# Kernel tuning notes

Hardware: AMD Instinct MI355X
Metric: run time of the kernel (lower is better)

Reference implementation:

```python
import jax, jax.numpy as jnp
import numpy as np

NUM_EMBEDDINGS = 1024
EMBEDDING_DIM = 128
COMMITMENT_COST = 0.25


def setup_inputs() -> dict:
    key = jax.random.key(0)
    k1, k2 = jax.random.split(key)
    z = jax.random.normal(k1, (16, EMBEDDING_DIM, 64, 64), dtype=jnp.float32)
    # torch init: uniform(-1/num_embeddings, 1/num_embeddings)
    lim = 1.0 / NUM_EMBEDDINGS
    embedding = jax.random.uniform(
        k2, (NUM_EMBEDDINGS, EMBEDDING_DIM), dtype=jnp.float32,
        minval=-lim, maxval=lim)
    return {"z": z, "embedding": embedding}


def reference(z, embedding):
    b, c, h, w = z.shape  # c == EMBEDDING_DIM
    # (b, h, w, c) -> (b*h*w, c)
    z_flat = jnp.transpose(z, (0, 2, 3, 1)).reshape(-1, c)
    # squared euclidean distances: ||z||^2 + ||e||^2 - 2 z e^T  -> (N, K)
    distances = (jnp.sum(z_flat ** 2, axis=-1, keepdims=True)
                 + jnp.sum(embedding ** 2, axis=-1)[None, :]
                 - 2.0 * jnp.matmul(z_flat, embedding.T))
    encoding_indices = jnp.argmin(distances, axis=-1)  # (N,) int
    z_q = embedding[encoding_indices].reshape(b, h, w, c)
    z_q = jnp.transpose(z_q, (0, 3, 1, 2))  # (b, c, h, w)
    commitment_loss = COMMITMENT_COST * jnp.sum(
        (jax.lax.stop_gradient(z_q) - z) ** 2)
    codebook_loss = jnp.sum((z_q - jax.lax.stop_gradient(z)) ** 2)
    loss = codebook_loss + commitment_loss
    # straight-through estimator
    z_q_st = z + jax.lax.stop_gradient(z_q - z)
    return (z_q_st, loss, encoding_indices, commitment_loss, codebook_loss)
```

## Files before the change

kernel.cpp:

```cpp
#include <hip/hip_runtime.h>
#include <hip/hip_bf16.h>

#define C 128
#define HW 4096
#define NPOS 65536
#define K 1024
#define MB 128
#define NBLK (NPOS/MB)
#define RS 136
#define RSB 272
#define CHK 64
#define NCH (K/CHK)
#define CHB (CHK*RSB)

#define ZQ_OFF 0
#define LOSS_OFF 8388608
#define IDX_OFF 8388609
#define COMMIT_OFF 8454145
#define CODE_OFF 8454146

#define WS_IMG_OFF 8192

typedef __bf16 bf16x8 __attribute__((ext_vector_type(8)));
typedef float f32x4 __attribute__((ext_vector_type(4)));

__global__ void vq_prep(const float* __restrict__ emb, unsigned char* __restrict__ img) {
    int k = blockIdx.x;
    int l = threadIdx.x;
    float v0 = emb[k * C + l];
    float v1 = emb[k * C + 64 + l];
    __hip_bfloat16 h0 = __float2bfloat16(v0);
    __hip_bfloat16 h1 = __float2bfloat16(v1);
    unsigned short* row = (unsigned short*)(img + (size_t)k * RSB);
    row[l] = *(unsigned short*)&h0;
    row[64 + l] = *(unsigned short*)&h1;
    float s = v0 * v0 + v1 * v1;
    #pragma unroll
    for (int off = 32; off; off >>= 1) s += __shfl_down(s, off);
    if (l == 0) *(float*)(img + (size_t)k * RSB + 256) = s + 1.0f;
}

__global__ __launch_bounds__(256, 2)
void vq_main(const float* __restrict__ z, const float* __restrict__ emb,
             const unsigned char* __restrict__ img,
             float* __restrict__ out, float* __restrict__ S) {
    __shared__ unsigned short zt[MB * RS];
    __shared__ unsigned short bbuf[2][CHK * RS];
    __shared__ unsigned int wbest[4][MB];
    __shared__ unsigned short idxs[MB];
    __shared__ float lred[4];

    const int t = threadIdx.x;
    const int w = t >> 6;
    const int lane = t & 63;
    const int nn = lane & 15;
    const int q = lane >> 4;

    const int blk = blockIdx.x;
    const int n0g = blk * MB;
    const int b = n0g >> 12;
    const int hw0 = n0g & (HW - 1);
    const float* zg = z + (size_t)b * C * HW + hw0;

    for (int j = w; j < 17; j += 4) {
        __builtin_amdgcn_global_load_lds(
            (const __attribute__((address_space(1))) unsigned int*)(img + j * 1024 + lane * 16),
            (__attribute__((address_space(3))) unsigned int*)((unsigned char*)bbuf[0] + j * 1024),
            16, 0, 0);
    }

    {
        int pos = t & (MB - 1);
        int c0b = (t >> 7) * 64;
        #pragma unroll
        for (int i = 0; i < 16; ++i) {
            int c0 = c0b + i * 4;
            float f0 = zg[(size_t)(c0 + 0) * HW + pos];
            float f1 = zg[(size_t)(c0 + 1) * HW + pos];
            float f2 = zg[(size_t)(c0 + 2) * HW + pos];
            float f3 = zg[(size_t)(c0 + 3) * HW + pos];
            __hip_bfloat16 h0 = __float2bfloat16(f0), h1 = __float2bfloat16(f1),
                           h2 = __float2bfloat16(f2), h3 = __float2bfloat16(f3);
            ushort4 pk;
            pk.x = *(unsigned short*)&h0; pk.y = *(unsigned short*)&h1;
            pk.z = *(unsigned short*)&h2; pk.w = *(unsigned short*)&h3;
            *(ushort4*)&zt[pos * RS + c0] = pk;
        }
    }
    __syncthreads();

    bf16x8 a[8][4];
    #pragma unroll
    for (int mt = 0; mt < 8; ++mt)
        #pragma unroll
        for (int ks = 0; ks < 4; ++ks)
            a[mt][ks] = *(bf16x8*)&zt[(mt * 16 + nn) * RS + ks * 32 + q * 8];

    unsigned int best[8][4];
    #pragma unroll
    for (int mt = 0; mt < 8; ++mt)
        #pragma unroll
        for (int r = 0; r < 4; ++r) best[mt][r] = 0xFFFFFFFFu;

    for (int ch = 0; ch < NCH; ++ch) {
        const int p = ch & 1;
        if (ch + 1 < NCH) {
            const unsigned char* src = img + (size_t)(ch + 1) * CHB;
            for (int j = w; j < 17; j += 4) {
                __builtin_amdgcn_global_load_lds(
                    (const __attribute__((address_space(1))) unsigned int*)(src + j * 1024 + lane * 16),
                    (__attribute__((address_space(3))) unsigned int*)((unsigned char*)bbuf[p ^ 1] + j * 1024),
                    16, 0, 0);
            }
        }
        const unsigned short* bb = bbuf[p];
        const int row = w * 16 + nn;
        bf16x8 bf[4];
        #pragma unroll
        for (int ks = 0; ks < 4; ++ks)
            bf[ks] = *(bf16x8*)&bb[row * RS + ks * 32 + q * 8];
        const float en1 = *(const float*)&bb[row * RS + 128];
        const unsigned int code = (unsigned int)(ch * CHK + row);

        f32x4 acc[8];
        #pragma unroll
        for (int mt = 0; mt < 8; ++mt) acc[mt] = (f32x4){0.f, 0.f, 0.f, 0.f};
        #pragma unroll
        for (int ks = 0; ks < 4; ++ks)
            #pragma unroll
            for (int mt = 0; mt < 8; ++mt)
                acc[mt] = __builtin_amdgcn_mfma_f32_16x16x32_bf16(a[mt][ks], bf[ks], acc[mt], 0, 0, 0);

        #pragma unroll
        for (int mt = 0; mt < 8; ++mt)
            #pragma unroll
            for (int r = 0; r < 4; ++r) {
                float s = fmaf(acc[mt][r], -2.0f, en1);
                unsigned int u = (__float_as_uint(s) & ~1023u) | code;
                best[mt][r] = min(best[mt][r], u);
            }
        __syncthreads();
    }

    #pragma unroll
    for (int mt = 0; mt < 8; ++mt)
        #pragma unroll
        for (int r = 0; r < 4; ++r) {
            unsigned int v = best[mt][r];
            v = min(v, (unsigned int)__shfl_xor((int)v, 1));
            v = min(v, (unsigned int)__shfl_xor((int)v, 2));
            v = min(v, (unsigned int)__shfl_xor((int)v, 4));
            v = min(v, (unsigned int)__shfl_xor((int)v, 8));
            if (nn == 0) wbest[w][mt * 16 + q * 4 + r] = v;
        }
    __syncthreads();

    if (t < MB) {
        unsigned int v = min(min(wbest[0][t], wbest[1][t]), min(wbest[2][t], wbest[3][t]));
        unsigned int code = v & 1023u;
        idxs[t] = (unsigned short)code;
        out[IDX_OFF + n0g + t] = (float)code;
    }
    __syncthreads();

    {
        int pos = t & (MB - 1);
        int c0b = (t >> 7) * 64;
        int myidx = idxs[pos];
        const float* erow = emb + (size_t)myidx * C;
        float* og = out + ZQ_OFF + (size_t)b * C * HW + hw0;
        float ls = 0.f;
        #pragma unroll
        for (int i = 0; i < 16; ++i) {
            int c0 = c0b + i * 4;
            float4 ev = *(const float4*)&erow[c0];
            ushort4 zz = *(ushort4*)&zt[pos * RS + c0];
            float z0 = __uint_as_float((unsigned int)zz.x << 16);
            float z1 = __uint_as_float((unsigned int)zz.y << 16);
            float z2 = __uint_as_float((unsigned int)zz.z << 16);
            float z3 = __uint_as_float((unsigned int)zz.w << 16);
            float d0 = z0 - ev.x, d1 = z1 - ev.y, d2 = z2 - ev.z, d3 = z3 - ev.w;
            ls += d0 * d0 + d1 * d1 + d2 * d2 + d3 * d3;
            og[(size_t)(c0 + 0) * HW + pos] = ev.x;
            og[(size_t)(c0 + 1) * HW + pos] = ev.y;
            og[(size_t)(c0 + 2) * HW + pos] = ev.z;
            og[(size_t)(c0 + 3) * HW + pos] = ev.w;
        }
        #pragma unroll
        for (int off = 32; off; off >>= 1) ls += __shfl_down(ls, off);
        if (lane == 0) lred[w] = ls;
    }
    __syncthreads();
    if (t == 0) atomicAdd(S, lred[0] + lred[1] + lred[2] + lred[3]);
}

__global__ void vq_final(const float* __restrict__ S, float* __restrict__ out) {
    float s = *S;
    out[LOSS_OFF] = 1.25f * s;
    out[COMMIT_OFF] = 0.25f * s;
    out[CODE_OFF] = s;
}

extern "C" void kernel_launch(void* const* d_in, const int* in_sizes, int n_in,
                              void* d_out, int out_size, void* d_ws, size_t ws_size,
                              hipStream_t stream) {
    const float* z = (const float*)d_in[0];
    const float* emb = (const float*)d_in[1];
    float* out = (float*)d_out;
    float* S = (float*)d_ws;
    unsigned char* img = (unsigned char*)d_ws + WS_IMG_OFF;

    hipMemsetAsync(d_ws, 0, 64, stream);
    vq_prep<<<K, 64, 0, stream>>>(emb, img);
    vq_main<<<NBLK, 256, 0, stream>>>(z, emb, img, out, S);
    vq_final<<<1, 1, 0, stream>>>(S, out);
}
```

Baseline: 118.5 us.

## Load codebook fragments directly into registers and fold finalize into main kernel

Each wave now reads its bf16 codebook fragments straight from global memory (L2-resident) into registers, with one-chunk-ahead register prefetch. This replaces the LDS double buffer, which needed a __syncthreads per chunk. Embedding norms move to a separate array, and the prep kernel is vectorized to handle 8 rows per block. The final loss kernel is removed: the last block, detected through an atomic counter, writes the loss scalars. The trade-off is more global/L2 traffic per wave, since every block's waves re-read the codebook, plus extra register pressure from the prefetch buffers.

```diff
diff --git a/kernel.cpp b/kernel.cpp
--- a/kernel.cpp
+++ b/kernel.cpp
@@ -8,10 +8,10 @@
 #define MB 128
 #define NBLK (NPOS/MB)
 #define RS 136
-#define RSB 272
 #define CHK 64
 #define NCH (K/CHK)
-#define CHB (CHK*RSB)
+#define IMG_RS 256
+#define CHB (CHK*IMG_RS)
 
 #define ZQ_OFF 0
 #define LOSS_OFF 8388608
@@ -19,33 +19,35 @@
 #define COMMIT_OFF 8454145
 #define CODE_OFF 8454146
 
+#define WS_EN_OFF 256
 #define WS_IMG_OFF 8192
 
 typedef __bf16 bf16x8 __attribute__((ext_vector_type(8)));
 typedef float f32x4 __attribute__((ext_vector_type(4)));
 
-__global__ void vq_prep(const float* __restrict__ emb, unsigned char* __restrict__ img) {
-    int k = blockIdx.x;
-    int l = threadIdx.x;
-    float v0 = emb[k * C + l];
-    float v1 = emb[k * C + 64 + l];
-    __hip_bfloat16 h0 = __float2bfloat16(v0);
-    __hip_bfloat16 h1 = __float2bfloat16(v1);
-    unsigned short* row = (unsigned short*)(img + (size_t)k * RSB);
-    row[l] = *(unsigned short*)&h0;
-    row[64 + l] = *(unsigned short*)&h1;
-    float s = v0 * v0 + v1 * v1;
-    #pragma unroll
-    for (int off = 32; off; off >>= 1) s += __shfl_down(s, off);
-    if (l == 0) *(float*)(img + (size_t)k * RSB + 256) = s + 1.0f;
+__global__ void vq_prep(const float* __restrict__ emb, unsigned char* __restrict__ img,
+                        float* __restrict__ enorm1) {
+    int t = threadIdx.x;
+    int r = t >> 5, l = t & 31;
+    int k = blockIdx.x * 8 + r;
+    float4 v = ((const float4*)emb)[k * 32 + l];
+    __hip_bfloat16 h0 = __float2bfloat16(v.x), h1 = __float2bfloat16(v.y),
+                   h2 = __float2bfloat16(v.z), h3 = __float2bfloat16(v.w);
+    ushort4 pk;
+    pk.x = *(unsigned short*)&h0; pk.y = *(unsigned short*)&h1;
+    pk.z = *(unsigned short*)&h2; pk.w = *(unsigned short*)&h3;
+    *(ushort4*)(img + (size_t)k * IMG_RS + l * 8) = pk;
+    float s = v.x * v.x + v.y * v.y + v.z * v.z + v.w * v.w;
+    #pragma unroll
+    for (int off = 16; off; off >>= 1) s += __shfl_xor(s, off);
+    if (l == 0) enorm1[k] = s + 1.0f;
 }
 
 __global__ __launch_bounds__(256, 2)
 void vq_main(const float* __restrict__ z, const float* __restrict__ emb,
-             const unsigned char* __restrict__ img,
-             float* __restrict__ out, float* __restrict__ S) {
+             const unsigned char* __restrict__ img, const float* __restrict__ enorm1,
+             float* __restrict__ out, float* __restrict__ S, unsigned int* __restrict__ cnt) {
     __shared__ unsigned short zt[MB * RS];
-    __shared__ unsigned short bbuf[2][CHK * RS];
     __shared__ unsigned int wbest[4][MB];
     __shared__ unsigned short idxs[MB];
     __shared__ float lred[4];
@@ -56,18 +58,10 @@
     const int nn = lane & 15;
     const int q = lane >> 4;
 
-    const int blk = blockIdx.x;
-    const int n0g = blk * MB;
+    const int n0g = blockIdx.x * MB;
     const int b = n0g >> 12;
     const int hw0 = n0g & (HW - 1);
     const float* zg = z + (size_t)b * C * HW + hw0;
-
-    for (int j = w; j < 17; j += 4) {
-        __builtin_amdgcn_global_load_lds(
-            (const __attribute__((address_space(1))) unsigned int*)(img + j * 1024 + lane * 16),
-            (__attribute__((address_space(3))) unsigned int*)((unsigned char*)bbuf[0] + j * 1024),
-            16, 0, 0);
-    }
 
     {
         int pos = t & (MB - 1);
@@ -102,25 +96,23 @@
         #pragma unroll
         for (int r = 0; r < 4; ++r) best[mt][r] = 0xFFFFFFFFu;
 
+    const unsigned char* gB = img + (size_t)(w * 16 + nn) * IMG_RS + q * 16;
+    const float* gE = enorm1 + w * 16 + nn;
+
+    bf16x8 bcur[4], bnxt[4];
+    #pragma unroll
+    for (int ks = 0; ks < 4; ++ks)
+        bcur[ks] = *(const bf16x8*)(gB + ks * 64);
+
     for (int ch = 0; ch < NCH; ++ch) {
-        const int p = ch & 1;
         if (ch + 1 < NCH) {
-            const unsigned char* src = img + (size_t)(ch + 1) * CHB;
-            for (int j = w; j < 17; j += 4) {
-                __builtin_amdgcn_global_load_lds(
-                    (const __attribute__((address_space(1))) unsigned int*)(src + j * 1024 + lane * 16),
-                    (__attribute__((address_space(3))) unsigned int*)((unsigned char*)bbuf[p ^ 1] + j * 1024),
-                    16, 0, 0);
-            }
-        }
-        const unsigned short* bb = bbuf[p];
-        const int row = w * 16 + nn;
-        bf16x8 bf[4];
-        #pragma unroll
-        for (int ks = 0; ks < 4; ++ks)
-            bf[ks] = *(bf16x8*)&bb[row * RS + ks * 32 + q * 8];
-        const float en1 = *(const float*)&bb[row * RS + 128];
-        const unsigned int code = (unsigned int)(ch * CHK + row);
+            const unsigned char* src = gB + (size_t)(ch + 1) * CHB;
+            #pragma unroll
+            for (int ks = 0; ks < 4; ++ks)
+                bnxt[ks] = *(const bf16x8*)(src + ks * 64);
+        }
+        const float en1 = gE[ch * CHK];
+        const unsigned int code = (unsigned int)(ch * CHK + w * 16 + nn);
 
         f32x4 acc[8];
         #pragma unroll
@@ -129,7 +121,7 @@
         for (int ks = 0; ks < 4; ++ks)
             #pragma unroll
             for (int mt = 0; mt < 8; ++mt)
-                acc[mt] = __builtin_amdgcn_mfma_f32_16x16x32_bf16(a[mt][ks], bf[ks], acc[mt], 0, 0, 0);
+                acc[mt] = __builtin_amdgcn_mfma_f32_16x16x32_bf16(a[mt][ks], bcur[ks], acc[mt], 0, 0, 0);
 
         #pragma unroll
         for (int mt = 0; mt < 8; ++mt)
@@ -139,7 +131,8 @@
                 unsigned int u = (__float_as_uint(s) & ~1023u) | code;
                 best[mt][r] = min(best[mt][r], u);
             }
-        __syncthreads();
+        #pragma unroll
+        for (int ks = 0; ks < 4; ++ks) bcur[ks] = bnxt[ks];
     }
 
     #pragma unroll
@@ -191,14 +184,18 @@
         if (lane == 0) lred[w] = ls;
     }
     __syncthreads();
-    if (t == 0) atomicAdd(S, lred[0] + lred[1] + lred[2] + lred[3]);
-}
-
-__global__ void vq_final(const float* __restrict__ S, float* __restrict__ out) {
-    float s = *S;
-    out[LOSS_OFF] = 1.25f * s;
-    out[COMMIT_OFF] = 0.25f * s;
-    out[CODE_OFF] = s;
+
+    if (t == 0) {
+        atomicAdd(S, lred[0] + lred[1] + lred[2] + lred[3]);
+        __threadfence();
+        unsigned int old = atomicAdd(cnt, 1u);
+        if (old == NBLK - 1) {
+            float s = atomicAdd(S, 0.0f);
+            out[LOSS_OFF] = 1.25f * s;
+            out[COMMIT_OFF] = 0.25f * s;
+            out[CODE_OFF] = s;
+        }
+    }
 }
 
 extern "C" void kernel_launch(void* const* d_in, const int* in_sizes, int n_in,
@@ -208,10 +205,11 @@
     const float* emb = (const float*)d_in[1];
     float* out = (float*)d_out;
     float* S = (float*)d_ws;
+    unsigned int* cnt = (unsigned int*)d_ws + 1;
+    float* enorm1 = (float*)((unsigned char*)d_ws + WS_EN_OFF);
     unsigned char* img = (unsigned char*)d_ws + WS_IMG_OFF;
 
     hipMemsetAsync(d_ws, 0, 64, stream);
-    vq_prep<<<K, 64, 0, stream>>>(emb, img);
-    vq_main<<<NBLK, 256, 0, stream>>>(z, emb, img, out, S);
-    vq_final<<<1, 1, 0, stream>>>(S, out);
+    vq_prep<<<K / 8, 256, 0, stream>>>(emb, img, enorm1);
+    vq_main<<<NBLK, 256, 0, stream>>>(z, emb, img, enorm1, out, S, cnt);
 }
```

Result: slower. 131.6 us (+11.0%).
